# Optimization experiments

Hardware: AMD Instinct MI355X
Metric: run time of the kernel (lower is better)

## Reference

```python
import jax, jax.numpy as jnp
import numpy as np

NHID, NHEAD, HEAD_DIM, U = 512, 16, 64, 3  # U = unfold_size (hardcoded 3 in original)
B, L = 8, 2048
D = NHEAD * HEAD_DIM  # 1024


def setup_inputs() -> dict:
    key = jax.random.key(0)
    ks = jax.random.split(key, 9)
    s = 0.02
    return {
        "x": jax.random.normal(ks[0], (B, NHID, L, 1), jnp.float32),
        "wq": jax.random.normal(ks[1], (NHID, D), jnp.float32) * s,
        "bq": jnp.zeros((D,), jnp.float32),
        "wk": jax.random.normal(ks[2], (NHID, D), jnp.float32) * s,
        "bk": jnp.zeros((D,), jnp.float32),
        "wv": jax.random.normal(ks[3], (NHID, D), jnp.float32) * s,
        "bv": jnp.zeros((D,), jnp.float32),
        "wo": jax.random.normal(ks[4], (D, NHID), jnp.float32) * s,
        "bo": jnp.zeros((NHID,), jnp.float32),
    }


def _unfold(t):
    # t: (B, D, L). Replicates tf.image.extract_patches (ksize 3, SAME, zero pad)
    # followed by the original's reshape (B,L,1,D,3) -- which reinterprets the
    # window-major flat layout (w*D + c) as (c', w') -- then transpose to
    # (B, D, 3, L) and reshape to (B, nhead, head_dim, 3, L).
    b, d, l = t.shape
    tt = jnp.transpose(t, (0, 2, 1))                  # (B, L, D)
    tp = jnp.pad(tt, ((0, 0), (1, 1), (0, 0)))        # SAME zero padding along L
    p = jnp.stack([tp[:, w:w + l, :] for w in range(U)], axis=2)  # (B, L, 3, D), flat idx = w*D + c
    p = p.reshape(b, l, d, U)                         # faithful reinterpreting reshape
    p = jnp.transpose(p, (0, 2, 3, 1))                # (B, D, 3, L)
    return p.reshape(b, NHEAD, HEAD_DIM, U, l)


def reference(x, wq, bq, wk, bk, wv, bv, wo, bo):
    b, c, l, _ = x.shape
    xs = x[..., 0]                                    # (B, C, L)
    # 1x1 convs (channels_first) == channel matmuls
    q = jnp.einsum('bcl,cd->bdl', xs, wq) + bq[None, :, None]
    k = jnp.einsum('bcl,cd->bdl', xs, wk) + bk[None, :, None]
    v = jnp.einsum('bcl,cd->bdl', xs, wv) + bv[None, :, None]
    q = q.reshape(b, NHEAD, HEAD_DIM, 1, l)           # (B, nh, hd, 1, L)
    k = _unfold(k)                                    # (B, nh, hd, 3, L)
    v = _unfold(v)
    scale = jnp.sqrt(jnp.asarray(HEAD_DIM, x.dtype))
    alphas = jnp.sum(q * k, axis=2, keepdims=True) / scale  # (B, nh, 1, 3, L)
    alphas = jax.nn.softmax(alphas, axis=3)
    att = jnp.sum(alphas * v, axis=3)                 # (B, nh, hd, L)
    # faithful to original: transpose then reinterpreting reshape to (B, D, L)
    att = jnp.transpose(att, (0, 1, 3, 2)).reshape(b, D, l)
    ret = jnp.einsum('bdl,dc->bcl', att, wo) + bo[None, :, None]
    return ret[..., None]                             # (B, nhid, L, 1)
```

## Files before the change

### kernel.cpp

```cpp
#include <hip/hip_runtime.h>

typedef _Float16 f16_t;
typedef _Float16 f16x2 __attribute__((ext_vector_type(2)));
typedef _Float16 f16x8 __attribute__((ext_vector_type(8)));
typedef float floatx4 __attribute__((ext_vector_type(4)));
typedef unsigned int u32;
typedef const __attribute__((address_space(1))) unsigned int* gptr_as1;
typedef __attribute__((address_space(3))) unsigned int* lptr_as3;

#define B_ 8
#define C_ 512
#define L_ 2048
#define D_ 1024
#define H_ 16

static __device__ __forceinline__ f16x2 bc2(u32 v) { return __builtin_bit_cast(f16x2, v); }
static __device__ __forceinline__ u32 cb2(f16x2 v) { return __builtin_bit_cast(u32, v); }

__global__ __launch_bounds__(256) void _MSA1_ktransf2h(const float* __restrict__ in,
                                                       f16_t* __restrict__ out,
                                                       int R, int C) {
  size_t zoff = (size_t)blockIdx.z * R * C;
  in += zoff; out += zoff;
  __shared__ f16_t tile[64][65];
  int r0 = blockIdx.y * 64, c0 = blockIdx.x * 64;
  int t = threadIdx.x;
  #pragma unroll
  for (int i = 0; i < 16; ++i) {
    int idx = t + i * 256;
    int r = idx >> 6, c = idx & 63;
    tile[c][r] = (f16_t)in[(size_t)(r0 + r) * C + (c0 + c)];
  }
  __syncthreads();
  #pragma unroll
  for (int i = 0; i < 16; ++i) {
    int idx = t + i * 256;
    int r = idx >> 6, c = idx & 63;
    out[(size_t)(c0 + r) * R + (r0 + c)] = tile[r][c];
  }
}

__global__ __launch_bounds__(256) void _MSA1_kprep(
    const float* __restrict__ wq, const float* __restrict__ wk,
    const float* __restrict__ wv, const float* __restrict__ wo,
    const float* __restrict__ bq, const float* __restrict__ bk,
    const float* __restrict__ bv,
    f16_t* __restrict__ wT3, f16_t* __restrict__ woT, float* __restrict__ bias3) {
  const int x = blockIdx.x, y = blockIdx.y;
  const int t = threadIdx.x;
  if (x == 128) {
    if (y == 0) {
      for (int i = t; i < 1024; i += 256) {
        bias3[i] = bq[i];
        bias3[1024 + i] = bk[i];
        bias3[2048 + i] = bv[i];
      }
    }
    return;
  }
  __shared__ f16_t tile[64][65];
  const float* in; f16_t* out; int R, C, r0, c0;
  if (y < 3) {
    R = 512; C = 1024;
    in = (y == 0) ? wq : (y == 1) ? wk : wv;
    out = wT3 + (size_t)y * 524288;
    r0 = (x >> 4) * 64; c0 = (x & 15) * 64;
  } else {
    R = 1024; C = 512;
    in = wo; out = woT;
    r0 = (x >> 3) * 64; c0 = (x & 7) * 64;
  }
  #pragma unroll
  for (int i = 0; i < 16; ++i) {
    int idx = t + i * 256;
    int r = idx >> 6, c = idx & 63;
    tile[c][r] = (f16_t)in[(size_t)(r0 + r) * C + (c0 + c)];
  }
  __syncthreads();
  #pragma unroll
  for (int i = 0; i < 16; ++i) {
    int idx = t + i * 256;
    int r = idx >> 6, c = idx & 63;
    out[(size_t)(c0 + r) * R + (r0 + c)] = tile[r][c];
  }
}

template <bool F32OUT, int K>
__global__ __launch_bounds__(256) void _MSA1_kgemm(
    const f16_t* __restrict__ A, const f16_t* __restrict__ Bt,
    const float* __restrict__ bias, void* __restrict__ Cdv,
    int M, int N, long sA, long sB, long sC) {
  A  += (size_t)blockIdx.z * sA;
  Bt += (size_t)blockIdx.z * sB;
  const int m0 = blockIdx.y * 128, n0 = blockIdx.x * 128;

  union ShU {
    struct { f16_t As[128][32]; f16_t Bs[128][32]; } ab;
    f16_t Ep[F32OUT ? 1 : 64][132];
  };
  __shared__ ShU sh;

  const int t = threadIdx.x;
  const int lane = t & 63, w = t >> 6;
  const int mh = (w & 1) * 64, nh = (w >> 1) * 64;
  const int fm = lane & 15, fq = lane >> 4;
  const int srcoff = ((t & 3) ^ ((t >> 2) & 3)) * 8;
  const int colf = ((fq ^ (fm & 3)) * 8);

  floatx4 acc[4][4];
  #pragma unroll
  for (int i = 0; i < 4; ++i)
    #pragma unroll
    for (int j = 0; j < 4; ++j) {
      floatx4 z4 = {0.f, 0.f, 0.f, 0.f};
      acc[i][j] = z4;
    }

  for (int kt = 0; kt < K; kt += 32) {
    __syncthreads();
    #pragma unroll
    for (int j = 0; j < 2; ++j) {
      int chunk = j * 256 + t;
      int r = chunk >> 2;
      const f16_t* ga = A + (size_t)(m0 + r) * K + kt + srcoff;
      __builtin_amdgcn_global_load_lds((gptr_as1)(const void*)ga,
          (lptr_as3)(void*)((char*)&sh.ab.As[0][0] + j * 4096 + w * 1024), 16, 0, 0);
      const f16_t* gb = Bt + (size_t)(n0 + r) * K + kt + srcoff;
      __builtin_amdgcn_global_load_lds((gptr_as1)(const void*)gb,
          (lptr_as3)(void*)((char*)&sh.ab.Bs[0][0] + j * 4096 + w * 1024), 16, 0, 0);
    }
    __syncthreads();

    f16x8 af[4], bfr[4];
    #pragma unroll
    for (int mt = 0; mt < 4; ++mt)
      af[mt] = *(const f16x8*)&sh.ab.As[mh + mt * 16 + fm][colf];
    #pragma unroll
    for (int nt = 0; nt < 4; ++nt)
      bfr[nt] = *(const f16x8*)&sh.ab.Bs[nh + nt * 16 + fm][colf];
    #pragma unroll
    for (int mt = 0; mt < 4; ++mt)
      #pragma unroll
      for (int nt = 0; nt < 4; ++nt)
        acc[mt][nt] = __builtin_amdgcn_mfma_f32_16x16x32_f16(
            af[mt], bfr[nt], acc[mt][nt], 0, 0, 0);
  }
  __syncthreads();

  if (F32OUT) {
    float* Cd = (float*)Cdv + (size_t)blockIdx.z * sC;
    #pragma unroll
    for (int mt = 0; mt < 4; ++mt) {
      float bv4[4];
      #pragma unroll
      for (int r = 0; r < 4; ++r)
        bv4[r] = bias[m0 + mh + mt * 16 + fq * 4 + r];
      #pragma unroll
      for (int nt = 0; nt < 4; ++nt) {
        int col = n0 + nh + nt * 16 + fm;
        #pragma unroll
        for (int r = 0; r < 4; ++r) {
          int row = m0 + mh + mt * 16 + fq * 4 + r;
          Cd[(size_t)row * N + col] = acc[mt][nt][r] + bv4[r];
        }
      }
    }
  } else {
    f16_t* Cd = (f16_t*)Cdv + (size_t)blockIdx.z * sC;
    #pragma unroll
    for (int half = 0; half < 2; ++half) {
      if (half) __syncthreads();
      if (mh == half * 64) {
        #pragma unroll
        for (int mt = 0; mt < 4; ++mt) {
          float bv4[4];
          #pragma unroll
          for (int r = 0; r < 4; ++r)
            bv4[r] = bias[m0 + half * 64 + mt * 16 + fq * 4 + r];
          #pragma unroll
          for (int nt = 0; nt < 4; ++nt) {
            int col = nh + nt * 16 + fm;
            #pragma unroll
            for (int r = 0; r < 4; ++r) {
              int row = mt * 16 + fq * 4 + r;
              sh.Ep[row][col] = (f16_t)(acc[mt][nt][r] + bv4[r]);
            }
          }
        }
      }
      __syncthreads();
      #pragma unroll
      for (int i = 0; i < 8; ++i) {
        int chunk = i * 256 + t;
        int row = chunk >> 5, c8 = chunk & 31;
        uint2 val = *(const uint2*)&sh.Ep[row][c8 * 4];
        *(uint2*)&Cd[(size_t)(m0 + half * 64 + row) * N + n0 + c8 * 4] = val;
      }
    }
  }
}

__global__ __launch_bounds__(256) void _MSA1_kattn6(const f16_t* __restrict__ qkv,
                                                    f16_t* __restrict__ attT) {
  const int t = threadIdx.x;
  const int lane = t & 63;
  const int wid = __builtin_amdgcn_readfirstlane(t >> 6);
  const int hb = blockIdx.x;
  const int h = hb & 15, b = hb >> 4;
  const int chi = blockIdx.y;
  const int lbase = chi * 256;
  const int l0 = lbase + lane * 4;
  const size_t plane = (size_t)D_ * L_;
  const f16_t* base = qkv + (size_t)b * 3 * plane;

  __shared__ uint2 sred[4][3][64];
  __shared__ __align__(16) f16_t tile2[2048][8];

  const f16_t* qp = base + (size_t)(h * 64 + wid * 16) * L_ + l0;
  const f16_t* kpl = base + plane;
  const f16_t* vpl = base + 2 * plane;
  const int g0 = h * 192 + wid * 48;

  f16x2 sLo[3], sHi[3];
  #pragma unroll
  for (int w = 0; w < 3; ++w) { f16x2 z = {(f16_t)0, (f16_t)0}; sLo[w] = z; sHi[w] = z; }

  #pragma unroll
  for (int dd = 0; dd < 16; ++dd) {
    uint2 qw = *(const uint2*)(qp + (size_t)dd * L_);
    f16x2 qlo = bc2(qw.x), qhi = bc2(qw.y);
    #pragma unroll
    for (int w = 0; w < 3; ++w) {
      int g = g0 + 3 * dd + w;
      int c = g & 1023;
      int o = (g >> 10) - 1;
      uint2 kw = *(const uint2*)(kpl + (size_t)c * L_ + (l0 + o));
      if (o < 0 && l0 == 0) kw.x &= 0xFFFF0000u;
      if (o > 0 && l0 == 2044) kw.y &= 0x0000FFFFu;
      sLo[w] = bc2(kw.x) * qlo + sLo[w];
      sHi[w] = bc2(kw.y) * qhi + sHi[w];
    }
  }
  #pragma unroll
  for (int w = 0; w < 3; ++w) {
    uint2 v; v.x = cb2(sLo[w]); v.y = cb2(sHi[w]);
    sred[wid][w][lane] = v;
  }
  __syncthreads();

  float sc[4][3];
  #pragma unroll
  for (int j = 0; j < 3; ++j) {
    uint2 r0 = sred[0][j][lane], r1 = sred[1][j][lane];
    uint2 r2 = sred[2][j][lane], r3 = sred[3][j][lane];
    f16x2 lo = (bc2(r0.x) + bc2(r1.x)) + (bc2(r2.x) + bc2(r3.x));
    f16x2 hi = (bc2(r0.y) + bc2(r1.y)) + (bc2(r2.y) + bc2(r3.y));
    sc[0][j] = (float)lo.x * 0.125f;
    sc[1][j] = (float)lo.y * 0.125f;
    sc[2][j] = (float)hi.x * 0.125f;
    sc[3][j] = (float)hi.y * 0.125f;
  }
  f16_t ef[4][3];
  #pragma unroll
  for (int li = 0; li < 4; ++li) {
    float mx = fmaxf(sc[li][0], fmaxf(sc[li][1], sc[li][2]));
    float e0 = __expf(sc[li][0] - mx), e1 = __expf(sc[li][1] - mx), e2 = __expf(sc[li][2] - mx);
    float inv = 1.f / (e0 + e1 + e2);
    ef[li][0] = (f16_t)(e0 * inv); ef[li][1] = (f16_t)(e1 * inv); ef[li][2] = (f16_t)(e2 * inv);
  }
  f16x2 eLo[3], eHi[3];
  #pragma unroll
  for (int w = 0; w < 3; ++w) {
    f16x2 a = {ef[0][w], ef[1][w]}; eLo[w] = a;
    f16x2 b2 = {ef[2][w], ef[3][w]}; eHi[w] = b2;
  }

  const int llb = (lane & 7) * 256 + wid * 16;
  const int jcol = lane >> 3;
  #pragma unroll
  for (int dd = 0; dd < 16; ++dd) {
    f16x2 aLo = {(f16_t)0, (f16_t)0}, aHi = {(f16_t)0, (f16_t)0};
    #pragma unroll
    for (int w = 0; w < 3; ++w) {
      int g = g0 + 3 * dd + w;
      int c = g & 1023;
      int o = (g >> 10) - 1;
      uint2 vw = *(const uint2*)(vpl + (size_t)c * L_ + (l0 + o));
      if (o < 0 && l0 == 0) vw.x &= 0xFFFF0000u;
      if (o > 0 && l0 == 2044) vw.y &= 0x0000FFFFu;
      aLo = bc2(vw.x) * eLo[w] + aLo;
      aHi = bc2(vw.y) * eHi[w] + aHi;
    }
    const int llq = llb + dd;
    tile2[llq +   0][jcol] = aLo.x;
    tile2[llq +  64][jcol] = aLo.y;
    tile2[llq + 128][jcol] = aHi.x;
    tile2[llq + 192][jcol] = aHi.y;
  }
  __syncthreads();

  f16_t* ob = attT + (size_t)b * L_ * D_ + h * 64 + chi * 8;
  #pragma unroll
  for (int i = 0; i < 8; ++i) {
    int ll = i * 256 + t;
    uint4 val = *(const uint4*)&tile2[ll][0];
    *(uint4*)(ob + (size_t)ll * D_) = val;
  }
}

extern "C" void kernel_launch(void* const* d_in, const int* in_sizes, int n_in,
                              void* d_out, int out_size, void* d_ws, size_t ws_size,
                              hipStream_t stream) {
  (void)in_sizes; (void)n_in; (void)out_size;
  const float* x  = (const float*)d_in[0];
  const float* wq = (const float*)d_in[1];
  const float* bq = (const float*)d_in[2];
  const float* wk = (const float*)d_in[3];
  const float* bk = (const float*)d_in[4];
  const float* wv = (const float*)d_in[5];
  const float* bv = (const float*)d_in[6];
  const float* wo = (const float*)d_in[7];
  const float* bo = (const float*)d_in[8];
  float* out = (float*)d_out;
  char* ws = (char*)d_ws;

  f16_t* wT3   = (f16_t*)(ws);
  f16_t* woT   = (f16_t*)(ws + 3145728);
  float* bias3 = (float*) (ws + 4194304);
  const size_t SHARED_END = 4210688;

  _MSA1_kprep<<<dim3(129, 4), dim3(256), 0, stream>>>(
      wq, wk, wv, wo, bq, bk, bv, wT3, woT, bias3);

  if (ws_size >= 155205632ull) {
    f16_t* xT    = (f16_t*)(ws + SHARED_END);
    f16_t* qkv   = xT + 8388608ull;
    f16_t* att2T = qkv + 50331648ull;

    _MSA1_ktransf2h<<<dim3(32, 8, B_), dim3(256), 0, stream>>>(x, xT, 512, 2048);
    _MSA1_kgemm<false, 512><<<dim3(16, 24, B_), dim3(256), 0, stream>>>(
        wT3, xT, bias3, qkv, 3072, 2048,
        0L, (long)(2048 * 512), (long)(3072 * 2048));
    _MSA1_kattn6<<<dim3(128, 8), dim3(256), 0, stream>>>(qkv, att2T);
    _MSA1_kgemm<true, 1024><<<dim3(16, 4, B_), dim3(256), 0, stream>>>(
        woT, att2T, bo, out, 512, 2048,
        0L, (long)(2048 * 1024), (long)(512 * 2048));
  } else {
    f16_t* xTb    = (f16_t*)(ws + SHARED_END);
    f16_t* qkvb   = xTb + 1048576ull;
    f16_t* att2Tb = qkvb + 6291456ull;
    for (int b = 0; b < B_; ++b) {
      const float* xb = x + (size_t)b * C_ * L_;
      _MSA1_ktransf2h<<<dim3(32, 8, 1), dim3(256), 0, stream>>>(xb, xTb, 512, 2048);
      _MSA1_kgemm<false, 512><<<dim3(16, 24, 1), dim3(256), 0, stream>>>(
          wT3, xTb, bias3, qkvb, 3072, 2048, 0L, 0L, 0L);
      _MSA1_kattn6<<<dim3(16, 8), dim3(256), 0, stream>>>(qkvb, att2Tb);
      _MSA1_kgemm<true, 1024><<<dim3(16, 4, 1), dim3(256), 0, stream>>>(
          woT, att2Tb, bo, out + (size_t)b * C_ * L_, 512, 2048, 0L, 0L, 0L);
    }
  }
}
```

Baseline: 270.8 us.

## Triple-buffer GEMM LDS tiles with async prefetch and single barrier per step

The GEMM main loop moves from single-buffered LDS staging with two barriers per k-step to a three-stage ring. Tiles are prefetched two steps ahead via global_load_lds, and each step uses partial vmcnt waits and one barrier. The LDS swizzle also gains an extra XOR term to reduce bank conflicts on the fragment reads. This targets exposed global-load latency, at the cost of three times the staging LDS, which may lower occupancy.

```diff
diff --git a/kernel.cpp b/kernel.cpp
--- a/kernel.cpp
+++ b/kernel.cpp
@@ -94,8 +94,8 @@
   Bt += (size_t)blockIdx.z * sB;
   const int m0 = blockIdx.y * 128, n0 = blockIdx.x * 128;
 
-  union ShU {
-    struct { f16_t As[128][32]; f16_t Bs[128][32]; } ab;
+  union __align__(16) ShU {
+    struct { f16_t As[3][128][32]; f16_t Bs[3][128][32]; } ab;
     f16_t Ep[F32OUT ? 1 : 64][132];
   };
   __shared__ ShU sh;
@@ -104,8 +104,8 @@
   const int lane = t & 63, w = t >> 6;
   const int mh = (w & 1) * 64, nh = (w >> 1) * 64;
   const int fm = lane & 15, fq = lane >> 4;
-  const int srcoff = ((t & 3) ^ ((t >> 2) & 3)) * 8;
-  const int colf = ((fq ^ (fm & 3)) * 8);
+  const int srcswz = ((t & 3) ^ ((t >> 2) & 3) ^ ((t >> 4) & 3)) * 8;
+  const int colf = ((fq ^ (fm & 3) ^ ((fm >> 2) & 3)) * 8);
 
   floatx4 acc[4][4];
   #pragma unroll
@@ -116,34 +116,56 @@
       acc[i][j] = z4;
     }
 
-  for (int kt = 0; kt < K; kt += 32) {
-    __syncthreads();
+  auto STAGE = [&](int kt, int bi) {
     #pragma unroll
     for (int j = 0; j < 2; ++j) {
       int chunk = j * 256 + t;
       int r = chunk >> 2;
-      const f16_t* ga = A + (size_t)(m0 + r) * K + kt + srcoff;
+      const f16_t* ga = A + (size_t)(m0 + r) * K + kt + srcswz;
       __builtin_amdgcn_global_load_lds((gptr_as1)(const void*)ga,
-          (lptr_as3)(void*)((char*)&sh.ab.As[0][0] + j * 4096 + w * 1024), 16, 0, 0);
-      const f16_t* gb = Bt + (size_t)(n0 + r) * K + kt + srcoff;
+          (lptr_as3)(void*)((char*)&sh.ab.As[bi][0][0] + j * 4096 + w * 1024), 16, 0, 0);
+      const f16_t* gb = Bt + (size_t)(n0 + r) * K + kt + srcswz;
       __builtin_amdgcn_global_load_lds((gptr_as1)(const void*)gb,
-          (lptr_as3)(void*)((char*)&sh.ab.Bs[0][0] + j * 4096 + w * 1024), 16, 0, 0);
-    }
-    __syncthreads();
-
+          (lptr_as3)(void*)((char*)&sh.ab.Bs[bi][0][0] + j * 4096 + w * 1024), 16, 0, 0);
+    }
+  };
+
+  STAGE(0, 0);
+  STAGE(32, 1);
+  __builtin_amdgcn_sched_barrier(0);
+  asm volatile("s_waitcnt vmcnt(4)" ::: "memory");
+  __builtin_amdgcn_s_barrier();
+  __builtin_amdgcn_sched_barrier(0);
+
+  int bcur = 0;
+  for (int kt = 0; kt < K; kt += 32) {
+    if (kt + 64 < K) {
+      int bi = bcur + 2; if (bi >= 3) bi -= 3;
+      STAGE(kt + 64, bi);
+    }
     f16x8 af[4], bfr[4];
     #pragma unroll
     for (int mt = 0; mt < 4; ++mt)
-      af[mt] = *(const f16x8*)&sh.ab.As[mh + mt * 16 + fm][colf];
+      af[mt] = *(const f16x8*)&sh.ab.As[bcur][mh + mt * 16 + fm][colf];
     #pragma unroll
     for (int nt = 0; nt < 4; ++nt)
-      bfr[nt] = *(const f16x8*)&sh.ab.Bs[nh + nt * 16 + fm][colf];
+      bfr[nt] = *(const f16x8*)&sh.ab.Bs[bcur][nh + nt * 16 + fm][colf];
     #pragma unroll
     for (int mt = 0; mt < 4; ++mt)
       #pragma unroll
       for (int nt = 0; nt < 4; ++nt)
         acc[mt][nt] = __builtin_amdgcn_mfma_f32_16x16x32_f16(
             af[mt], bfr[nt], acc[mt][nt], 0, 0, 0);
+    if (kt + 32 < K) {
+      __builtin_amdgcn_sched_barrier(0);
+      if (kt + 64 < K)
+        asm volatile("s_waitcnt vmcnt(4) lgkmcnt(0)" ::: "memory");
+      else
+        asm volatile("s_waitcnt vmcnt(0) lgkmcnt(0)" ::: "memory");
+      __builtin_amdgcn_s_barrier();
+      __builtin_amdgcn_sched_barrier(0);
+    }
+    bcur = (bcur == 2) ? 0 : bcur + 1;
   }
   __syncthreads();
 
```

Result: no change. 265.8 us (-1.9%).
